# Kernel optimization log

Hardware: AMD Instinct MI355X
Metric: run time of the kernel (lower is better)

Reference implementation:

```python
import jax, jax.numpy as jnp
import numpy as np

N_EV, N_OBJ, D = 50000, 100000, 256
E1, E2 = 400000, 800000


def _ln(x, g, b):
    m = x.mean(-1, keepdims=True)
    v = x.var(-1, keepdims=True)
    return (x - m) * jax.lax.rsqrt(v + 1e-5) * g + b


def _lrelu(x):
    return jax.nn.leaky_relu(x, 0.2)


def setup_inputs():
    key = jax.random.key(0)
    ks = jax.random.split(key, 24)
    s = 1.0 / np.sqrt(D)
    W = lambda i, shp: (jax.random.normal(ks[i], shp, jnp.float32) * s)
    inp = {
        'object_X': jax.random.normal(ks[0], (N_OBJ, D), jnp.float32),
        'event_X': jax.random.normal(ks[1], (N_EV, D), jnp.float32),
        'Wo': W(2, (D, D)), 'bo': jnp.zeros((D,), jnp.float32),
        'go': jnp.ones((D,), jnp.float32), 'bon': jnp.zeros((D,), jnp.float32),
        'We': W(3, (D, D)), 'be': jnp.zeros((D,), jnp.float32),
        'ge': jnp.ones((D,), jnp.float32), 'ben': jnp.zeros((D,), jnp.float32),
        'Wu': W(4, (D, D)), 'bu': jnp.zeros((D,), jnp.float32),
        'Wl': W(5, (D, D)), 'bl': jnp.zeros((D,), jnp.float32),
        'g1': jnp.ones((D,), jnp.float32), 'b1': jnp.zeros((D,), jnp.float32),
        'g2': jnp.ones((D,), jnp.float32), 'b2': jnp.zeros((D,), jnp.float32),
        'Wh1': W(6, (D, D)), 'ah1': W(7, (2 * D,)),
        'Wh2': W(8, (D, D)), 'ah2': W(9, (2 * D,)),
        'oe_ev': jax.random.randint(ks[10], (E1,), 0, N_EV, jnp.int32),
        'oe_obj': jax.random.randint(ks[11], (E1,), 0, N_OBJ, jnp.int32),
        'hg_node': jax.random.randint(ks[12], (E2,), 0, N_EV + N_OBJ, jnp.int32),
        'hg_edge': jax.random.randint(ks[13], (E2,), 0, N_EV, jnp.int32),
        'total_events': N_EV,
    }
    return inp


def reference(object_X, event_X, Wo, bo, go, bon, We, be, ge, ben,
              Wu, bu, Wl, bl, g1, b1, g2, b2, Wh1, ah1, Wh2, ah2,
              oe_ev, oe_obj, hg_node, hg_edge, total_events):
    # proj chains (Dropout is identity at eval)
    obj = _ln(_lrelu(object_X @ Wo + bo), go, bon)
    ev = _ln(_lrelu(event_X @ We + be), ge, ben)
    # ObjectStateUpdater: aggregate incident-event features per object, project
    msg = jax.ops.segment_sum(ev[oe_ev], oe_obj, num_segments=N_OBJ)
    obj1 = _ln(_lrelu(msg @ Wu + bu) + obj, g1, b1)
    # LifecycleStateUpdater: linear lifecycle state transition
    obj2 = _ln(_lrelu(obj1 @ Wl + bl) + obj1, g2, b2)
    X = jnp.concatenate([ev, obj2], axis=0)  # [N_EV+N_OBJ, D]
    n_nodes = N_EV + N_OBJ

    def hgnn(X, W, a):
        m = (X @ W)[hg_node]  # [E2, D] gathered node messages
        cnt = jax.ops.segment_sum(jnp.ones((E2,), X.dtype), hg_edge, num_segments=total_events)
        ef = jax.ops.segment_sum(m, hg_edge, num_segments=total_events) / jnp.maximum(cnt, 1.0)[:, None]
        gth = ef[hg_edge]  # [E2, D] hyperedge feature per incidence
        score = _lrelu(m @ a[:D] + gth @ a[D:])  # [E2]
        smax = jax.ops.segment_max(score, hg_node, num_segments=n_nodes)
        e = jnp.exp(score - smax[hg_node])
        z = jax.ops.segment_sum(e, hg_node, num_segments=n_nodes)
        attn = e / jnp.maximum(z, 1e-9)[hg_node]
        out = jax.ops.segment_sum(attn[:, None] * gth, hg_node, num_segments=n_nodes)
        return _lrelu(out), attn

    h, _ = hgnn(X, Wh1, ah1)
    h, attn = hgnn(h, Wh2, ah2)  # layer-2 attention is what get_attention_weights() returns
    return (h, attn)
```

## Files before the change

kernel.cpp:

```cpp
#include <hip/hip_runtime.h>
#include <cstdio>

typedef __attribute__((ext_vector_type(8))) short short8_t;
typedef __attribute__((ext_vector_type(8))) unsigned short ushort8_t;
typedef __attribute__((ext_vector_type(4))) unsigned short us4;
typedef __attribute__((ext_vector_type(4))) float f32x4;

__device__ __forceinline__ unsigned short f2bf(float f) {
  unsigned u = __float_as_uint(f);
  u = u + 0x7FFFu + ((u >> 16) & 1u);
  return (unsigned short)(u >> 16);
}
__device__ __forceinline__ float bf2f(unsigned short h) {
  return __uint_as_float((unsigned)h << 16);
}
__device__ __forceinline__ float lrelu(float x) { return x > 0.f ? x : 0.2f * x; }

__global__ void k_pack_w6(const float* __restrict__ W0, const float* __restrict__ W1,
                          const float* __restrict__ W2, const float* __restrict__ W3,
                          const float* __restrict__ W4, const float* __restrict__ W5,
                          unsigned short* __restrict__ WF) {
  int which = blockIdx.x >> 8, k = blockIdx.x & 255, n = threadIdx.x;
  const float* W = which == 0 ? W0 : which == 1 ? W1 : which == 2 ? W2
                 : which == 3 ? W3 : which == 4 ? W4 : W5;
  int nt = n >> 4, l16 = n & 15;
  int ks = k >> 5, quad = (k >> 3) & 3, j = k & 7;
  size_t idx = ((size_t)which << 16) + (size_t)(((nt * 8 + ks) * 64 + quad * 16 + l16) * 8 + j);
  WF[idx] = f2bf(W[k * 256 + n]);
}


__global__ void k_count3(const int* __restrict__ hg_node, const int* __restrict__ hg_edge,
                         const int* __restrict__ oe_obj, int* __restrict__ cn,
                         int* __restrict__ ce, int* __restrict__ co, int nE2, int nE1) {
  int e = blockIdx.x * blockDim.x + threadIdx.x;
  if (e < nE2) {
    atomicAdd(&cn[hg_node[e]], 1);
    atomicAdd(&ce[hg_edge[e]], 1);
  }
  if (e < nE1) atomicAdd(&co[oe_obj[e]], 1);
}

__global__ void k_fill3(const int* __restrict__ hg_node, const int* __restrict__ hg_edge,
                        const int* __restrict__ oe_ev, const int* __restrict__ oe_obj,
                        const int* __restrict__ NS, const int* __restrict__ ES,
                        const int* __restrict__ OS, int* __restrict__ curn,
                        int* __restrict__ cure, int* __restrict__ curo,
                        int2* __restrict__ PE, int* __restrict__ NDe, int* __restrict__ EVo,
                        int nE2, int nE1) {
  int e = blockIdx.x * blockDim.x + threadIdx.x;
  if (e < nE2) {
    int sn = hg_node[e], se = hg_edge[e];
    int pn = NS[sn] + atomicAdd(&curn[sn], 1);
    PE[pn] = make_int2(e, se);
    int pe = ES[se] + atomicAdd(&cure[se], 1);
    NDe[pe] = sn;
  }
  if (e < nE1) {
    int so = oe_obj[e];
    int po = OS[so] + atomicAdd(&curo[so], 1);
    EVo[po] = oe_ev[e];
  }
}

__global__ __launch_bounds__(1024) void k_scan3(const int* __restrict__ c0, int* __restrict__ s0,
                                                int n0, const int* __restrict__ c1,
                                                int* __restrict__ s1, int n1,
                                                const int* __restrict__ c2, int* __restrict__ s2,
                                                int n2) {
  const int* cnt;
  int* starts;
  int n;
  if (blockIdx.x == 0) { cnt = c0; starts = s0; n = n0; }
  else if (blockIdx.x == 1) { cnt = c1; starts = s1; n = n1; }
  else { cnt = c2; starts = s2; n = n2; }
  __shared__ int wsum[16];
  int tid = threadIdx.x, lane = tid & 63, w = tid >> 6;
  int carry = 0;
  for (int base = 0; base < n; base += 4096) {
    int i0 = base + tid * 4;
    int4 c = make_int4(0, 0, 0, 0);
    if (i0 + 3 < n) c = *(const int4*)(cnt + i0);
    else {
      if (i0 < n) c.x = cnt[i0];
      if (i0 + 1 < n) c.y = cnt[i0 + 1];
      if (i0 + 2 < n) c.z = cnt[i0 + 2];
      if (i0 + 3 < n) c.w = cnt[i0 + 3];
    }
    int tsum = c.x + c.y + c.z + c.w;
    int inc = tsum;
    for (int o = 1; o < 64; o <<= 1) {
      int v = __shfl_up(inc, o);
      if (lane >= o) inc += v;
    }
    if (lane == 63) wsum[w] = inc;
    __syncthreads();
    int woff = 0;
    for (int k = 0; k < w; k++) woff += wsum[k];
    int excl = carry + woff + inc - tsum;
    if (i0 < n) starts[i0] = excl;
    if (i0 + 1 < n) starts[i0 + 1] = excl + c.x;
    if (i0 + 2 < n) starts[i0 + 2] = excl + c.x + c.y;
    if (i0 + 3 < n) starts[i0 + 3] = excl + c.x + c.y + c.z;
    int total = 0;
    for (int k = 0; k < 16; k++) total += wsum[k];
    carry += total;
    __syncthreads();
  }
  if (tid == 0) starts[n] = carry;
}

template <int HAS_SKIP, int A_F32>
__global__ __launch_bounds__(256) void k_gemm_ln(const void* __restrict__ Av,
                                                 const unsigned short* __restrict__ WF,
                                                 const float* __restrict__ bias,
                                                 const float* __restrict__ gamma,
                                                 const float* __restrict__ beta,
                                                 const unsigned short* skip,
                                                 unsigned short* outb, int rows, int nTiles) {
  __shared__ float red[2][4][16][2];
  int tid = threadIdx.x;
  int wave = tid >> 6, lane = tid & 63;
  int quad = lane >> 4, l16 = lane & 15;
  int buf = 0;
  for (int t = blockIdx.x; t < nTiles; t += gridDim.x, buf ^= 1) {
    size_t row0 = (size_t)t * 16;
    size_t arow = row0 + l16;
    short8_t af[8];
    if (A_F32) {
      bool inr = arow < (size_t)rows;
      const float4* ap = (const float4*)((const float*)Av + arow * 256);
#pragma unroll
      for (int ks = 0; ks < 8; ks++) {
        float4 f0 = make_float4(0.f, 0.f, 0.f, 0.f), f1 = f0;
        if (inr) {
          f0 = ap[ks * 8 + quad * 2];
          f1 = ap[ks * 8 + quad * 2 + 1];
        }
        ushort8_t a;
        a[0] = f2bf(f0.x); a[1] = f2bf(f0.y); a[2] = f2bf(f0.z); a[3] = f2bf(f0.w);
        a[4] = f2bf(f1.x); a[5] = f2bf(f1.y); a[6] = f2bf(f1.z); a[7] = f2bf(f1.w);
        af[ks] = (short8_t)a;
      }
    } else {
      const ushort8_t* ap = (const ushort8_t*)((const unsigned short*)Av + arow * 256);
#pragma unroll
      for (int ks = 0; ks < 8; ks++) af[ks] = (short8_t)ap[ks * 4 + quad];
    }

    f32x4 acc[4];
#pragma unroll
    for (int i = 0; i < 4; i++) acc[i] = (f32x4){0.f, 0.f, 0.f, 0.f};
#pragma unroll
    for (int ks = 0; ks < 8; ks++) {
#pragma unroll
      for (int c = 0; c < 4; c++) {
        int nt = wave * 4 + c;
        short8_t bf = *(const short8_t*)&WF[(size_t)(((nt * 8 + ks) * 64 + lane) * 8)];
        acc[c] = __builtin_amdgcn_mfma_f32_16x16x32_bf16(af[ks], bf, acc[c], 0, 0, 0);
      }
    }

    size_t rbase = row0 + quad * 4;
    float s[4] = {0, 0, 0, 0}, q[4] = {0, 0, 0, 0};
#pragma unroll
    for (int c = 0; c < 4; c++) {
      int col = (wave * 4 + c) * 16 + l16;
      float bv = bias[col];
#pragma unroll
      for (int r = 0; r < 4; r++) {
        float x = lrelu(acc[c][r] + bv);
        if (HAS_SKIP) {
          if (rbase + r < (size_t)rows) x += bf2f(skip[(rbase + r) * 256 + col]);
        }
        acc[c][r] = x;
        s[r] += x;
        q[r] += x * x;
      }
    }
#pragma unroll
    for (int o = 1; o < 16; o <<= 1)
#pragma unroll
      for (int r = 0; r < 4; r++) {
        s[r] += __shfl_xor(s[r], o);
        q[r] += __shfl_xor(q[r], o);
      }
    if (l16 == 0) {
#pragma unroll
      for (int r = 0; r < 4; r++) {
        red[buf][wave][quad * 4 + r][0] = s[r];
        red[buf][wave][quad * 4 + r][1] = q[r];
      }
    }
    __syncthreads();
    float mr[4], rs[4];
#pragma unroll
    for (int r = 0; r < 4; r++) {
      int row = quad * 4 + r;
      float S = red[buf][0][row][0] + red[buf][1][row][0] + red[buf][2][row][0] +
                red[buf][3][row][0];
      float Q = red[buf][0][row][1] + red[buf][1][row][1] + red[buf][2][row][1] +
                red[buf][3][row][1];
      float m = S * (1.f / 256.f);
      float v = Q * (1.f / 256.f) - m * m;
      mr[r] = m;
      rs[r] = rsqrtf(v + 1e-5f);
    }
#pragma unroll
    for (int c = 0; c < 4; c++) {
      int col = (wave * 4 + c) * 16 + l16;
      float g = gamma[col], bb = beta[col];
#pragma unroll
      for (int r = 0; r < 4; r++) {
        if (rbase + r < (size_t)rows) {
          float y = (acc[c][r] - mr[r]) * rs[r] * g + bb;
          outb[(rbase + r) * 256 + col] = f2bf(y);
        }
      }
    }
  }
}

__global__ __launch_bounds__(256) void k_gemm_xw(unsigned short* A,
                                                 const unsigned short* __restrict__ WF,
                                                 const float* __restrict__ a1,
                                                 float* __restrict__ s1, int rows,
                                                 int nTiles) {
  __shared__ float red[2][4][16];
  int tid = threadIdx.x;
  int wave = tid >> 6, lane = tid & 63;
  int quad = lane >> 4, l16 = lane & 15;
  int buf = 0;
  for (int t = blockIdx.x; t < nTiles; t += gridDim.x, buf ^= 1) {
    size_t row0 = (size_t)t * 16;
    size_t arow = row0 + l16;
    short8_t af[8];
    const ushort8_t* ap = (const ushort8_t*)(A + arow * 256);
#pragma unroll
    for (int ks = 0; ks < 8; ks++) af[ks] = (short8_t)ap[ks * 4 + quad];

    f32x4 acc[4];
#pragma unroll
    for (int i = 0; i < 4; i++) acc[i] = (f32x4){0.f, 0.f, 0.f, 0.f};
#pragma unroll
    for (int ks = 0; ks < 8; ks++) {
#pragma unroll
      for (int c = 0; c < 4; c++) {
        int nt = wave * 4 + c;
        short8_t bf = *(const short8_t*)&WF[(size_t)(((nt * 8 + ks) * 64 + lane) * 8)];
        acc[c] = __builtin_amdgcn_mfma_f32_16x16x32_bf16(af[ks], bf, acc[c], 0, 0, 0);
      }
    }

    size_t rbase = row0 + quad * 4;
    float s[4] = {0, 0, 0, 0};
#pragma unroll
    for (int c = 0; c < 4; c++) {
      float av = a1[(wave * 4 + c) * 16 + l16];
#pragma unroll
      for (int r = 0; r < 4; r++) s[r] += acc[c][r] * av;
    }
#pragma unroll
    for (int o = 1; o < 16; o <<= 1)
#pragma unroll
      for (int r = 0; r < 4; r++) s[r] += __shfl_xor(s[r], o);
    if (l16 == 0) {
#pragma unroll
      for (int r = 0; r < 4; r++) red[buf][wave][quad * 4 + r] = s[r];
    }
    __syncthreads();
#pragma unroll
    for (int c = 0; c < 4; c++) {
      int col = (wave * 4 + c) * 16 + l16;
#pragma unroll
      for (int r = 0; r < 4; r++)
        if (rbase + r < (size_t)rows) A[(rbase + r) * 256 + col] = f2bf(acc[c][r]);
    }
    if (wave == 0 && l16 == 0) {
#pragma unroll
      for (int r = 0; r < 4; r++) {
        int row = quad * 4 + r;
        if (rbase + r < (size_t)rows) {
          s1[rbase + r] = red[buf][0][row] + red[buf][1][row] + red[buf][2][row] +
                          red[buf][3][row];
        }
      }
    }
  }
}


__global__ __launch_bounds__(256) void k_edge_gather(const unsigned short* __restrict__ XW,
                                                     const int* __restrict__ ES,
                                                     const int* __restrict__ NDe,
                                                     const float* __restrict__ a2,
                                                     unsigned short* __restrict__ EF,
                                                     float* __restrict__ s2, int nEdges) {
  int wave = threadIdx.x >> 6, lane = threadIdx.x & 63;
  int r = blockIdx.x * 4 + wave;
  if (r >= nEdges) return;
  int s = ES[r], e = ES[r + 1];
  int cnt = e - s;
  float4 acc = make_float4(0.f, 0.f, 0.f, 0.f);
  if (cnt <= 64) {
    int myn = 0;
    if (lane < cnt) myn = NDe[s + lane];
    for (int base = 0; base < cnt; base += 8) {
      us4 u[8];
      float f[8];
#pragma unroll
      for (int t = 0; t < 8; t++) {
        int j2 = base + t;
        int n1 = __shfl(myn, j2);
        u[t] = ((const us4*)(XW + (size_t)n1 * 256))[lane];
        f[t] = (j2 < cnt) ? 1.f : 0.f;
      }
#pragma unroll
      for (int t = 0; t < 8; t++) {
        acc.x += f[t] * bf2f(u[t].x);
        acc.y += f[t] * bf2f(u[t].y);
        acc.z += f[t] * bf2f(u[t].z);
        acc.w += f[t] * bf2f(u[t].w);
      }
    }
  } else {
    for (int j = s; j < e; j++) {
      int n = NDe[j];
      us4 u = ((const us4*)(XW + (size_t)n * 256))[lane];
      acc.x += bf2f(u.x); acc.y += bf2f(u.y);
      acc.z += bf2f(u.z); acc.w += bf2f(u.w);
    }
  }
  float inv = 1.f / (float)(cnt > 1 ? cnt : 1);
  acc.x *= inv; acc.y *= inv; acc.z *= inv; acc.w *= inv;
  us4 ub = {f2bf(acc.x), f2bf(acc.y), f2bf(acc.z), f2bf(acc.w)};
  ((us4*)(EF + (size_t)r * 256))[lane] = ub;
  float4 a = ((const float4*)a2)[lane];
  float d = acc.x * a.x + acc.y * a.y + acc.z * a.z + acc.w * a.w;
  for (int o = 32; o; o >>= 1) d += __shfl_xor(d, o);
  if (lane == 0) s2[r] = d;
}

template <int WRITE_ATTN>
__global__ __launch_bounds__(256) void k_node_gather(const int* __restrict__ NS,
                                                     const int2* __restrict__ PE,
                                                     const float* __restrict__ s1,
                                                     const float* __restrict__ s2,
                                                     const unsigned short* __restrict__ EF,
                                                     unsigned short* outb, float* outf,
                                                     float* attn_out, int nNodes) {
  int wave = threadIdx.x >> 6, lane = threadIdx.x & 63;
  int n = blockIdx.x * 4 + wave;
  if (n >= nNodes) return;
  int s = NS[n], e = NS[n + 1];
  int cnt = e - s;
  float s1n = s1[n];
  float4 acc = make_float4(0.f, 0.f, 0.f, 0.f);
  if (cnt <= 64) {
    int mye0 = 0, myed = 0;
    float myscore = -3.4e38f;
    bool act = lane < cnt;
    if (act) {
      int2 pe = PE[s + lane];
      mye0 = pe.x;
      myed = pe.y;
      myscore = lrelu(s1n + s2[myed]);
    }
    float mymax = myscore;
    for (int o = 32; o; o >>= 1) mymax = fmaxf(mymax, __shfl_xor(mymax, o));
    float myexp = act ? __expf(myscore - mymax) : 0.f;
    float mysum = myexp;
    for (int o = 32; o; o >>= 1) mysum += __shfl_xor(mysum, o);
    float zinv = 1.f / fmaxf(mysum, 1e-9f);
    float myw = myexp * zinv;
    if (WRITE_ATTN && act) attn_out[mye0] = myw;
    for (int base = 0; base < cnt; base += 8) {
      us4 v[8];
      float w[8];
#pragma unroll
      for (int t = 0; t < 8; t++) {
        int j2 = base + t;
        int ed = __shfl(myed, j2);
        w[t] = __shfl(myw, j2);
        v[t] = ((const us4*)(EF + (size_t)ed * 256))[lane];
      }
#pragma unroll
      for (int t = 0; t < 8; t++) {
        acc.x += w[t] * bf2f(v[t].x);
        acc.y += w[t] * bf2f(v[t].y);
        acc.z += w[t] * bf2f(v[t].z);
        acc.w += w[t] * bf2f(v[t].w);
      }
    }
  } else {
    float mymax = -3.4e38f;
    for (int j = s + lane; j < e; j += 64) {
      mymax = fmaxf(mymax, lrelu(s1n + s2[PE[j].y]));
    }
    for (int o = 32; o; o >>= 1) mymax = fmaxf(mymax, __shfl_xor(mymax, o));
    float mysum = 0.f;
    for (int j = s + lane; j < e; j += 64) {
      mysum += __expf(lrelu(s1n + s2[PE[j].y]) - mymax);
    }
    for (int o = 32; o; o >>= 1) mysum += __shfl_xor(mysum, o);
    float zinv = 1.f / fmaxf(mysum, 1e-9f);
    for (int j = s; j < e; j++) {
      int2 pe = PE[j];
      float w = __expf(lrelu(s1n + s2[pe.y]) - mymax) * zinv;
      if (WRITE_ATTN) {
        if (lane == 0) attn_out[pe.x] = w;
      }
      us4 v = ((const us4*)(EF + (size_t)pe.y * 256))[lane];
      acc.x += w * bf2f(v.x); acc.y += w * bf2f(v.y);
      acc.z += w * bf2f(v.z); acc.w += w * bf2f(v.w);
    }
  }
  acc.x = lrelu(acc.x); acc.y = lrelu(acc.y);
  acc.z = lrelu(acc.z); acc.w = lrelu(acc.w);
  if (outb) {
    us4 u = {f2bf(acc.x), f2bf(acc.y), f2bf(acc.z), f2bf(acc.w)};
    ((us4*)(outb + (size_t)n * 256))[lane] = u;
  } else {
    ((float4*)(outf + (size_t)n * 256))[lane] = acc;
  }
}

__global__ __launch_bounds__(256) void k_obj_gather(const unsigned short* __restrict__ EVB,
                                                    const int* __restrict__ OS,
                                                    const int* __restrict__ EVo,
                                                    unsigned short* __restrict__ outb,
                                                    int nObj) {
  int wave = threadIdx.x >> 6, lane = threadIdx.x & 63;
  int o = blockIdx.x * 4 + wave;
  if (o >= nObj) return;
  int s = OS[o], e = OS[o + 1];
  int cnt = e - s;
  float4 acc = make_float4(0.f, 0.f, 0.f, 0.f);
  if (cnt <= 64) {
    int myev = 0;
    if (lane < cnt) myev = EVo[s + lane];
    for (int base = 0; base < cnt; base += 8) {
      us4 u[8];
      float f[8];
#pragma unroll
      for (int t = 0; t < 8; t++) {
        int j2 = base + t;
        int v1 = __shfl(myev, j2);
        u[t] = ((const us4*)(EVB + (size_t)v1 * 256))[lane];
        f[t] = (j2 < cnt) ? 1.f : 0.f;
      }
#pragma unroll
      for (int t = 0; t < 8; t++) {
        acc.x += f[t] * bf2f(u[t].x);
        acc.y += f[t] * bf2f(u[t].y);
        acc.z += f[t] * bf2f(u[t].z);
        acc.w += f[t] * bf2f(u[t].w);
      }
    }
  } else {
    for (int j = s; j < e; j++) {
      int ev = EVo[j];
      us4 u = ((const us4*)(EVB + (size_t)ev * 256))[lane];
      acc.x += bf2f(u.x); acc.y += bf2f(u.y);
      acc.z += bf2f(u.z); acc.w += bf2f(u.w);
    }
  }
  us4 u = {f2bf(acc.x), f2bf(acc.y), f2bf(acc.z), f2bf(acc.w)};
  ((us4*)(outb + (size_t)o * 256))[lane] = u;
}


extern "C" void kernel_launch(void* const* d_in, const int* in_sizes, int n_in,
                              void* d_out, int out_size, void* d_ws, size_t ws_size,
                              hipStream_t stream) {
  (void)n_in; (void)out_size;
  const float* object_X = (const float*)d_in[0];
  const float* event_X = (const float*)d_in[1];
  const float* Wo = (const float*)d_in[2];   const float* bo = (const float*)d_in[3];
  const float* go = (const float*)d_in[4];   const float* bon = (const float*)d_in[5];
  const float* We = (const float*)d_in[6];   const float* be = (const float*)d_in[7];
  const float* ge = (const float*)d_in[8];   const float* ben = (const float*)d_in[9];
  const float* Wu = (const float*)d_in[10];  const float* bu = (const float*)d_in[11];
  const float* Wl = (const float*)d_in[12];  const float* bl = (const float*)d_in[13];
  const float* g1 = (const float*)d_in[14];  const float* b1 = (const float*)d_in[15];
  const float* g2 = (const float*)d_in[16];  const float* b2 = (const float*)d_in[17];
  const float* Wh1 = (const float*)d_in[18]; const float* ah1 = (const float*)d_in[19];
  const float* Wh2 = (const float*)d_in[20]; const float* ah2 = (const float*)d_in[21];
  const int* oe_ev = (const int*)d_in[22];
  const int* oe_obj = (const int*)d_in[23];
  const int* hg_node = (const int*)d_in[24];
  const int* hg_edge = (const int*)d_in[25];

  const int N_OBJ = in_sizes[0] / 256;
  const int N_EV = in_sizes[1] / 256;
  const int E1 = in_sizes[22];
  const int E2 = in_sizes[24];
  const int NN = N_EV + N_OBJ;
  const int MEV = ((N_EV + 63) / 64) * 64;
  const int MOB = ((N_OBJ + 63) / 64) * 64;
  const int MX = ((NN + 63) / 64) * 64;
  const int EMX = E2 > E1 ? E2 : E1;
  const int TEV = MEV / 16, TOB = MOB / 16, TX = MX / 16;
  auto gsz = [](int t) { return t < 2048 ? t : 2048; };

  char* p = (char*)d_ws;
  auto take = [&](size_t bytes) {
    char* r = p;
    p += (bytes + 255) & ~(size_t)255;
    return r;
  };
  unsigned short* WF = (unsigned short*)take((size_t)6 * 65536 * 2);
  unsigned short* XBF = (unsigned short*)take((size_t)MX * 256 * 2);
  unsigned short* SB = (unsigned short*)take((size_t)MOB * 256 * 2);
  unsigned short* EF = SB;
  float* S1 = (float*)take((size_t)NN * 4);
  float* S2 = (float*)take((size_t)N_EV * 4);
  int* NS = (int*)take((size_t)(NN + 1) * 4);
  int* ES = (int*)take((size_t)(N_EV + 1) * 4);
  int* OS = (int*)take((size_t)(N_OBJ + 1) * 4);
  int* CNTn = (int*)take((size_t)NN * 4);
  int* CNTe = (int*)take((size_t)N_EV * 4);
  int* CNTo = (int*)take((size_t)N_OBJ * 4);
  int2* PEn = (int2*)take((size_t)E2 * 8);
  int* NDe = (int*)take((size_t)E2 * 4);
  int* EVo = (int*)take((size_t)E1 * 4);
  size_t need = (size_t)(p - (char*)d_ws);
  if (need > ws_size)
    fprintf(stderr, "[kernel_launch] WS OVERFLOW: need=%zu have=%zu\n", need, ws_size);

  float* out = (float*)d_out;
  unsigned short* OBJB = (unsigned short*)d_out;

  k_pack_w6<<<6 * 256, 256, 0, stream>>>(We, Wo, Wu, Wl, Wh1, Wh2, WF);

  if (MX > NN)
    hipMemsetAsync(XBF + (size_t)NN * 256, 0, (size_t)(MX - NN) * 512, stream);

  size_t cnt_span = (size_t)((char*)PEn - (char*)CNTn);
  hipMemsetAsync(CNTn, 0, cnt_span, stream);
  k_count3<<<(EMX + 255) / 256, 256, 0, stream>>>(hg_node, hg_edge, oe_obj, CNTn, CNTe, CNTo,
                                                  E2, E1);
  k_scan3<<<3, 1024, 0, stream>>>(CNTn, NS, NN, CNTe, ES, N_EV, CNTo, OS, N_OBJ);
  hipMemsetAsync(CNTn, 0, cnt_span, stream);
  k_fill3<<<(EMX + 255) / 256, 256, 0, stream>>>(hg_node, hg_edge, oe_ev, oe_obj, NS, ES, OS,
                                                 CNTn, CNTe, CNTo, PEn, NDe, EVo, E2, E1);

  k_gemm_ln<0, 1><<<gsz(TEV), 256, 0, stream>>>(event_X, WF + 0 * 65536, be, ge, ben, nullptr,
                                                XBF, N_EV, TEV);
  k_gemm_ln<0, 1><<<gsz(TOB), 256, 0, stream>>>(object_X, WF + 1 * 65536, bo, go, bon, nullptr,
                                                OBJB, N_OBJ, TOB);
  k_obj_gather<<<(N_OBJ + 3) / 4, 256, 0, stream>>>(XBF, OS, EVo, SB, N_OBJ);
  k_gemm_ln<1, 0><<<gsz(TOB), 256, 0, stream>>>(SB, WF + 2 * 65536, bu, g1, b1, OBJB, SB,
                                                N_OBJ, TOB);
  k_gemm_ln<1, 0><<<gsz(TOB), 256, 0, stream>>>(SB, WF + 3 * 65536, bl, g2, b2, SB,
                                                XBF + (size_t)N_EV * 256, N_OBJ, TOB);

  k_gemm_xw<<<gsz(TX), 256, 0, stream>>>(XBF, WF + 4 * 65536, ah1, S1, NN, TX);
  k_edge_gather<<<(N_EV + 3) / 4, 256, 0, stream>>>(XBF, ES, NDe, ah1 + 256, EF, S2, N_EV);
  k_node_gather<0><<<(NN + 3) / 4, 256, 0, stream>>>(NS, PEn, S1, S2, EF, XBF, nullptr,
                                                     nullptr, NN);
  k_gemm_xw<<<gsz(TX), 256, 0, stream>>>(XBF, WF + 5 * 65536, ah2, S1, NN, TX);
  k_edge_gather<<<(N_EV + 3) / 4, 256, 0, stream>>>(XBF, ES, NDe, ah2 + 256, EF, S2, N_EV);
  k_node_gather<1><<<(NN + 3) / 4, 256, 0, stream>>>(NS, PEn, S1, S2, EF, nullptr, out,
                                                     out + (size_t)NN * 256, NN);
}
```

Baseline: 1.206 ms.

## Fuse CSR count/fill into projection GEMM launches and record atomic ranks

Measured after the change: 1.148 ms. 1.05x faster.

```diff
diff --git a/kernel.cpp b/kernel.cpp
--- a/kernel.cpp
+++ b/kernel.cpp
@@ -30,37 +30,40 @@
 }
 
 
-__global__ void k_count3(const int* __restrict__ hg_node, const int* __restrict__ hg_edge,
-                         const int* __restrict__ oe_obj, int* __restrict__ cn,
-                         int* __restrict__ ce, int* __restrict__ co, int nE2, int nE1) {
-  int e = blockIdx.x * blockDim.x + threadIdx.x;
+__device__ __forceinline__ void count_body(int b, const int* __restrict__ hg_node,
+                                           const int* __restrict__ hg_edge,
+                                           const int* __restrict__ oe_obj,
+                                           int* __restrict__ cn, int* __restrict__ ce,
+                                           int* __restrict__ co, int* __restrict__ rkn,
+                                           int* __restrict__ rke, int* __restrict__ rko,
+                                           int nE2, int nE1) {
+  int e = b * 256 + (int)threadIdx.x;
   if (e < nE2) {
-    atomicAdd(&cn[hg_node[e]], 1);
-    atomicAdd(&ce[hg_edge[e]], 1);
-  }
-  if (e < nE1) atomicAdd(&co[oe_obj[e]], 1);
-}
-
-__global__ void k_fill3(const int* __restrict__ hg_node, const int* __restrict__ hg_edge,
-                        const int* __restrict__ oe_ev, const int* __restrict__ oe_obj,
-                        const int* __restrict__ NS, const int* __restrict__ ES,
-                        const int* __restrict__ OS, int* __restrict__ curn,
-                        int* __restrict__ cure, int* __restrict__ curo,
-                        int2* __restrict__ PE, int* __restrict__ NDe, int* __restrict__ EVo,
-                        int nE2, int nE1) {
-  int e = blockIdx.x * blockDim.x + threadIdx.x;
+    rkn[e] = atomicAdd(&cn[hg_node[e]], 1);
+    rke[e] = atomicAdd(&ce[hg_edge[e]], 1);
+  }
+  if (e < nE1) rko[e] = atomicAdd(&co[oe_obj[e]], 1);
+}
+
+__device__ __forceinline__ void fill_body(int b, const int* __restrict__ hg_node,
+                                          const int* __restrict__ hg_edge,
+                                          const int* __restrict__ oe_ev,
+                                          const int* __restrict__ oe_obj,
+                                          const int* __restrict__ NS,
+                                          const int* __restrict__ ES,
+                                          const int* __restrict__ OS,
+                                          const int* __restrict__ rkn,
+                                          const int* __restrict__ rke,
+                                          const int* __restrict__ rko,
+                                          int2* __restrict__ PE, int* __restrict__ NDe,
+                                          int* __restrict__ EVo, int nE2, int nE1) {
+  int e = b * 256 + (int)threadIdx.x;
   if (e < nE2) {
     int sn = hg_node[e], se = hg_edge[e];
-    int pn = NS[sn] + atomicAdd(&curn[sn], 1);
-    PE[pn] = make_int2(e, se);
-    int pe = ES[se] + atomicAdd(&cure[se], 1);
-    NDe[pe] = sn;
-  }
-  if (e < nE1) {
-    int so = oe_obj[e];
-    int po = OS[so] + atomicAdd(&curo[so], 1);
-    EVo[po] = oe_ev[e];
-  }
+    PE[NS[sn] + rkn[e]] = make_int2(e, se);
+    NDe[ES[se] + rke[e]] = sn;
+  }
+  if (e < nE1) EVo[OS[oe_obj[e]] + rko[e]] = oe_ev[e];
 }
 
 __global__ __launch_bounds__(1024) void k_scan3(const int* __restrict__ c0, int* __restrict__ s0,
@@ -111,19 +114,19 @@
 }
 
 template <int HAS_SKIP, int A_F32>
-__global__ __launch_bounds__(256) void k_gemm_ln(const void* __restrict__ Av,
-                                                 const unsigned short* __restrict__ WF,
-                                                 const float* __restrict__ bias,
-                                                 const float* __restrict__ gamma,
-                                                 const float* __restrict__ beta,
-                                                 const unsigned short* skip,
-                                                 unsigned short* outb, int rows, int nTiles) {
+__device__ __forceinline__ void gemm_ln_body(int bid, int G, const void* __restrict__ Av,
+                                             const unsigned short* __restrict__ WF,
+                                             const float* __restrict__ bias,
+                                             const float* __restrict__ gamma,
+                                             const float* __restrict__ beta,
+                                             const unsigned short* skip,
+                                             unsigned short* outb, int rows, int nTiles) {
   __shared__ float red[2][4][16][2];
   int tid = threadIdx.x;
   int wave = tid >> 6, lane = tid & 63;
   int quad = lane >> 4, l16 = lane & 15;
   int buf = 0;
-  for (int t = blockIdx.x; t < nTiles; t += gridDim.x, buf ^= 1) {
+  for (int t = bid; t < nTiles; t += G, buf ^= 1) {
     size_t row0 = (size_t)t * 16;
     size_t arow = row0 + l16;
     short8_t af[8];
@@ -219,6 +222,49 @@
       }
     }
   }
+}
+
+template <int HAS_SKIP, int A_F32>
+__global__ __launch_bounds__(256) void k_gemm_ln(const void* __restrict__ Av,
+                                                 const unsigned short* __restrict__ WF,
+                                                 const float* __restrict__ bias,
+                                                 const float* __restrict__ gamma,
+                                                 const float* __restrict__ beta,
+                                                 const unsigned short* skip,
+                                                 unsigned short* outb, int rows, int nTiles) {
+  gemm_ln_body<HAS_SKIP, A_F32>(blockIdx.x, gridDim.x, Av, WF, bias, gamma, beta, skip,
+                                outb, rows, nTiles);
+}
+
+__global__ __launch_bounds__(256) void k_gemm_count(
+    const void* __restrict__ Av, const unsigned short* __restrict__ WF,
+    const float* __restrict__ bias, const float* __restrict__ gamma,
+    const float* __restrict__ beta, unsigned short* outb, int rows, int nTiles, int CB,
+    int G, const int* __restrict__ hg_node, const int* __restrict__ hg_edge,
+    const int* __restrict__ oe_obj, int* cn, int* ce, int* co, int* rkn, int* rke, int* rko,
+    int nE2, int nE1) {
+  int b = blockIdx.x;
+  if (b < CB)
+    count_body(b, hg_node, hg_edge, oe_obj, cn, ce, co, rkn, rke, rko, nE2, nE1);
+  else
+    gemm_ln_body<0, 1>(b - CB, G, Av, WF, bias, gamma, beta, nullptr, outb, rows, nTiles);
+}
+
+__global__ __launch_bounds__(256) void k_gemm_fill(
+    const void* __restrict__ Av, const unsigned short* __restrict__ WF,
+    const float* __restrict__ bias, const float* __restrict__ gamma,
+    const float* __restrict__ beta, unsigned short* outb, int rows, int nTiles, int CB,
+    int G, const int* __restrict__ hg_node, const int* __restrict__ hg_edge,
+    const int* __restrict__ oe_ev, const int* __restrict__ oe_obj,
+    const int* __restrict__ NS, const int* __restrict__ ES, const int* __restrict__ OS,
+    const int* __restrict__ rkn, const int* __restrict__ rke, const int* __restrict__ rko,
+    int2* PE, int* NDe, int* EVo, int nE2, int nE1) {
+  int b = blockIdx.x;
+  if (b < CB)
+    fill_body(b, hg_node, hg_edge, oe_ev, oe_obj, NS, ES, OS, rkn, rke, rko, PE, NDe, EVo,
+              nE2, nE1);
+  else
+    gemm_ln_body<0, 1>(b - CB, G, Av, WF, bias, gamma, beta, nullptr, outb, rows, nTiles);
 }
 
 __global__ __launch_bounds__(256) void k_gemm_xw(unsigned short* A,
@@ -502,6 +548,7 @@
   const int EMX = E2 > E1 ? E2 : E1;
   const int TEV = MEV / 16, TOB = MOB / 16, TX = MX / 16;
   auto gsz = [](int t) { return t < 2048 ? t : 2048; };
+  const int CB = (EMX + 255) / 256;
 
   char* p = (char*)d_ws;
   auto take = [&](size_t bytes) {
@@ -521,6 +568,9 @@
   int* CNTn = (int*)take((size_t)NN * 4);
   int* CNTe = (int*)take((size_t)N_EV * 4);
   int* CNTo = (int*)take((size_t)N_OBJ * 4);
+  int* RKn = (int*)take((size_t)E2 * 4);
+  int* RKe = (int*)take((size_t)E2 * 4);
+  int* RKo = (int*)take((size_t)E1 * 4);
   int2* PEn = (int2*)take((size_t)E2 * 8);
   int* NDe = (int*)take((size_t)E2 * 4);
   int* EVo = (int*)take((size_t)E1 * 4);
@@ -536,19 +586,24 @@
   if (MX > NN)
     hipMemsetAsync(XBF + (size_t)NN * 256, 0, (size_t)(MX - NN) * 512, stream);
 
-  size_t cnt_span = (size_t)((char*)PEn - (char*)CNTn);
+  size_t cnt_span = (size_t)((char*)RKn - (char*)CNTn);
   hipMemsetAsync(CNTn, 0, cnt_span, stream);
-  k_count3<<<(EMX + 255) / 256, 256, 0, stream>>>(hg_node, hg_edge, oe_obj, CNTn, CNTe, CNTo,
-                                                  E2, E1);
+
+  {
+    int G = gsz(TEV);
+    k_gemm_count<<<CB + G, 256, 0, stream>>>(event_X, WF + 0 * 65536, be, ge, ben, XBF,
+                                             N_EV, TEV, CB, G, hg_node, hg_edge, oe_obj,
+                                             CNTn, CNTe, CNTo, RKn, RKe, RKo, E2, E1);
+  }
   k_scan3<<<3, 1024, 0, stream>>>(CNTn, NS, NN, CNTe, ES, N_EV, CNTo, OS, N_OBJ);
-  hipMemsetAsync(CNTn, 0, cnt_span, stream);
-  k_fill3<<<(EMX + 255) / 256, 256, 0, stream>>>(hg_node, hg_edge, oe_ev, oe_obj, NS, ES, OS,
-                                                 CNTn, CNTe, CNTo, PEn, NDe, EVo, E2, E1);
-
-  k_gemm_ln<0, 1><<<gsz(TEV), 256, 0, stream>>>(event_X, WF + 0 * 65536, be, ge, ben, nullptr,
-                                                XBF, N_EV, TEV);
-  k_gemm_ln<0, 1><<<gsz(TOB), 256, 0, stream>>>(object_X, WF + 1 * 65536, bo, go, bon, nullptr,
-                                                OBJB, N_OBJ, TOB);
+  {
+    int G = gsz(TOB);
+    k_gemm_fill<<<CB + G, 256, 0, stream>>>(object_X, WF + 1 * 65536, bo, go, bon, OBJB,
+                                            N_OBJ, TOB, CB, G, hg_node, hg_edge, oe_ev,
+                                            oe_obj, NS, ES, OS, RKn, RKe, RKo, PEn, NDe,
+                                            EVo, E2, E1);
+  }
+
   k_obj_gather<<<(N_OBJ + 3) / 4, 256, 0, stream>>>(XBF, OS, EVo, SB, N_OBJ);
   k_gemm_ln<1, 0><<<gsz(TOB), 256, 0, stream>>>(SB, WF + 2 * 65536, bu, g1, b1, OBJB, SB,
                                                 N_OBJ, TOB);
```
